# Kernel tuning notes

Hardware: AMD Instinct MI355X
Metric: run time of the kernel (lower is better)

Reference implementation:

```python
import jax, jax.numpy as jnp
import numpy as np

OUT_CHANNELS = 16
PH = PW = 7          # output_size
SR = 2               # sampling_ratio


def setup_inputs() -> dict:
    key = jax.random.key(0)
    k1, k2, k3, k4 = jax.random.split(key, 4)
    B, C, H, W = 4, OUT_CHANNELS * PH * PW, 80, 80
    feat = jax.random.normal(k1, (B, C, H, W), dtype=jnp.float32)
    N = 512
    bidx = jax.random.randint(k2, (N,), 0, B).astype(jnp.float32)
    tl = jax.random.uniform(k3, (N, 2), minval=0.0, maxval=0.7)   # x1, y1 (normalized)
    sz = jax.random.uniform(k4, (N, 2), minval=0.05, maxval=0.3)  # box size
    rois = jnp.concatenate([bidx[:, None], tl, tl + sz], axis=1)  # [N,5]
    return {"input": feat, "rois": rois}


def _psroi_one(feat_ps, roi):
    # feat_ps: [B, Co, PH, PW, H, W]  (position-sensitive channel layout)
    B, Co, _, _, H, W = feat_ps.shape
    f = feat_ps[roi[0].astype(jnp.int32)]              # [Co, PH, PW, H, W]
    x1 = roi[1] * W; y1 = roi[2] * H
    x2 = roi[3] * W; y2 = roi[4] * H                   # adaptive spatial_scale = (H, W)
    roi_h = jnp.maximum(y2 - y1, 0.1)
    roi_w = jnp.maximum(x2 - x1, 0.1)
    bin_h = roi_h / PH
    bin_w = roi_w / PW
    # sample coordinates per bin: [PH,SR] and [PW,SR]
    ys = y1 + jnp.arange(PH, dtype=f.dtype)[:, None] * bin_h + (jnp.arange(SR, dtype=f.dtype)[None, :] + 0.5) * bin_h / SR
    xs = x1 + jnp.arange(PW, dtype=f.dtype)[:, None] * bin_w + (jnp.arange(SR, dtype=f.dtype)[None, :] + 0.5) * bin_w / SR
    ym = (ys >= -1.0) & (ys <= H)
    xm = (xs >= -1.0) & (xs <= W)
    yc = jnp.clip(ys, 0.0, H - 1)
    xc = jnp.clip(xs, 0.0, W - 1)
    y0 = jnp.floor(yc).astype(jnp.int32)
    x0 = jnp.floor(xc).astype(jnp.int32)
    y1i = jnp.minimum(y0 + 1, H - 1)
    x1i = jnp.minimum(x0 + 1, W - 1)
    ly = yc - y0.astype(f.dtype); hy = 1.0 - ly        # [PH,SR]
    lx = xc - x0.astype(f.dtype); hx = 1.0 - lx        # [PW,SR]
    I = jnp.arange(PH)[:, None, None, None]            # bin row index
    J = jnp.arange(PW)[None, None, :, None]            # bin col index

    def g(Y, X):
        # gather f[c, i, j, Y[i,sy], X[j,sx]] -> [Co, PH, SR, PW, SR]
        return f[:, I, J, Y[:, :, None, None], X[None, None, :, :]]

    v = (g(y0, x0)  * (hy[:, :, None, None] * hx[None, None])
       + g(y0, x1i) * (hy[:, :, None, None] * lx[None, None])
       + g(y1i, x0) * (ly[:, :, None, None] * hx[None, None])
       + g(y1i, x1i) * (ly[:, :, None, None] * lx[None, None]))
    v = v * (ym[:, :, None, None] & xm[None, None]).astype(v.dtype)
    return v.mean(axis=(2, 4))                          # [Co, PH, PW]


def reference(input, rois):
    B, C, H, W = input.shape
    feat_ps = input.reshape(B, OUT_CHANNELS, PH, PW, H, W)
    rois = rois.reshape(-1, 5)
    out = jax.vmap(lambda r: _psroi_one(feat_ps, r))(rois)  # [N, Co, PH, PW]
    return out
```

## Files before the change

kernel.cpp:

```cpp
#include <hip/hip_runtime.h>

#define NB   4
#define CO   16
#define PH   7
#define PW   7
#define SR   2
#define HH   80
#define WW   80
#define NROI 512
#define CIJ  (CO*PH*PW)
#define PLANE (HH*WW)
#define NF4  (PLANE/4)

typedef float f4v __attribute__((ext_vector_type(4), aligned(16)));

#define WS_ORDER_OFF 64
#define WS_GEOM_OFF  2048

__global__ __launch_bounds__(512) void psroi_prep_kernel(
    const float* __restrict__ rois, int* __restrict__ base,
    unsigned short* __restrict__ order, f4v* __restrict__ geom)
{
    __shared__ int cnt[NB];
    __shared__ int cbase[NB + 1];
    int n = threadIdx.x;
    if (n < NB) cnt[n] = 0;
    __syncthreads();
    int b = (int)rois[n * 5 + 0];
    int rank = atomicAdd(&cnt[b], 1);
    __syncthreads();
    if (n == 0) {
        cbase[0] = 0;
        for (int k = 0; k < NB; ++k) cbase[k + 1] = cbase[k] + cnt[k];
        for (int k = 0; k <= NB; ++k) base[k] = cbase[k];
    }
    __syncthreads();
    int pos = cbase[b] + rank;
    order[pos] = (unsigned short)n;

    float x1 = rois[n * 5 + 1] * (float)WW;
    float y1 = rois[n * 5 + 2] * (float)HH;
    float x2 = rois[n * 5 + 3] * (float)WW;
    float y2 = rois[n * 5 + 4] * (float)HH;
    f4v g;
    g.x = x1;
    g.y = y1;
    g.z = fmaxf(x2 - x1, 0.1f) * (1.0f / PW);
    g.w = fmaxf(y2 - y1, 0.1f) * (1.0f / PH);
    geom[pos] = g;
}

__global__ __launch_bounds__(256) void psroi_main_kernel(
    const float* __restrict__ feat,
    const int* __restrict__ base,
    const unsigned short* __restrict__ order,
    const f4v* __restrict__ geom,
    float* __restrict__ out)
{
    __shared__ __align__(16) float sp[PLANE];

    int u   = blockIdx.x;
    int cij = u >> 2;
    int b   = u & 3;
    int rem = cij % (PH * PW);
    int i = rem / PW;
    int j = rem % PW;
    int n = threadIdx.x;

    const f4v* src = (const f4v*)(feat + ((size_t)b * CIJ + (size_t)cij) * PLANE);
    f4v* dst = (f4v*)sp;
    #pragma unroll
    for (int it = 0; it < 6; ++it)
        dst[it * 256 + n] = src[it * 256 + n];
    {
        int e = 1536 + n;
        if (e < NF4) dst[e] = src[e];
    }

    int lo = base[b];
    int hi = base[b + 1];

    __syncthreads();

    for (int t = lo + n; t < hi; t += 256) {
        int m = (int)order[t];
        f4v g = geom[t];
        float x1 = g.x, y1 = g.y, bin_w = g.z, bin_h = g.w;

        float acc = 0.0f;
        #pragma unroll
        for (int sy = 0; sy < SR; ++sy) {
            float ys = y1 + (float)i * bin_h + ((float)sy + 0.5f) * bin_h / (float)SR;
            bool ymask = (ys >= -1.0f) && (ys <= (float)HH);
            float yc = fminf(fmaxf(ys, 0.0f), (float)(HH - 1));
            int   y0 = (int)floorf(yc);
            int   y1i = min(y0 + 1, HH - 1);
            float ly = yc - (float)y0, hy = 1.0f - ly;
            #pragma unroll
            for (int sx = 0; sx < SR; ++sx) {
                float xs = x1 + (float)j * bin_w + ((float)sx + 0.5f) * bin_w / (float)SR;
                bool xmask = (xs >= -1.0f) && (xs <= (float)WW);
                float xc = fminf(fmaxf(xs, 0.0f), (float)(WW - 1));
                int   x0 = (int)floorf(xc);
                int   x0c = min(x0, WW - 2);
                bool  sh = (x0 != x0c);
                float lx = xc - (float)x0, hx = 1.0f - lx;

                float t0 = sp[y0  * WW + x0c], t1 = sp[y0  * WW + x0c + 1];
                float b0 = sp[y1i * WW + x0c], b1 = sp[y1i * WW + x0c + 1];

                float v00 = sh ? t1 : t0;
                float v10 = sh ? b1 : b0;
                float v = (v00 * hx + t1 * lx) * hy + (v10 * hx + b1 * lx) * ly;
                if (ymask && xmask) acc += v;
            }
        }
        out[(size_t)m * CIJ + cij] = acc * 0.25f;
    }
}

extern "C" void kernel_launch(void* const* d_in, const int* in_sizes, int n_in,
                              void* d_out, int out_size, void* d_ws, size_t ws_size,
                              hipStream_t stream)
{
    const float* feat = (const float*)d_in[0];
    const float* rois = (const float*)d_in[1];
    float* out = (float*)d_out;

    char* ws = (char*)d_ws;
    int* base = (int*)ws;
    unsigned short* order = (unsigned short*)(ws + WS_ORDER_OFF);
    f4v* geom = (f4v*)(ws + WS_GEOM_OFF);

    psroi_prep_kernel<<<1, NROI, 0, stream>>>(rois, base, order, geom);
    psroi_main_kernel<<<CIJ * NB, 256, 0, stream>>>(feat, base, order, geom, out);
}
```

Baseline: 112.3 us.

## Drop ROI bucketing prep kernel; each block scans all ROIs and filters by batch

Removes the separate prep kernel that sorted ROIs by batch index and precomputed geometry, so the whole operation is one launch. Each block now has every thread read two ROIs directly, compute geometry inline, and skip ROIs whose batch does not match the block's batch. This saves a kernel launch and the serialization between the two kernels. In exchange every block reads all 512 ROIs, and lanes whose ROI belongs to another batch sit idle, causing warp divergence.

```diff
diff --git a/kernel.cpp b/kernel.cpp
--- a/kernel.cpp
+++ b/kernel.cpp
@@ -14,47 +14,52 @@
 
 typedef float f4v __attribute__((ext_vector_type(4), aligned(16)));
 
-#define WS_ORDER_OFF 64
-#define WS_GEOM_OFF  2048
+__device__ __forceinline__ void psroi_one(
+    const float* __restrict__ sp,
+    float rb, float rx1, float ry1, float rx2, float ry2,
+    int b, int i, int j, int cij, int m, float* __restrict__ out)
+{
+    if ((int)rb != b) return;
 
-__global__ __launch_bounds__(512) void psroi_prep_kernel(
-    const float* __restrict__ rois, int* __restrict__ base,
-    unsigned short* __restrict__ order, f4v* __restrict__ geom)
-{
-    __shared__ int cnt[NB];
-    __shared__ int cbase[NB + 1];
-    int n = threadIdx.x;
-    if (n < NB) cnt[n] = 0;
-    __syncthreads();
-    int b = (int)rois[n * 5 + 0];
-    int rank = atomicAdd(&cnt[b], 1);
-    __syncthreads();
-    if (n == 0) {
-        cbase[0] = 0;
-        for (int k = 0; k < NB; ++k) cbase[k + 1] = cbase[k] + cnt[k];
-        for (int k = 0; k <= NB; ++k) base[k] = cbase[k];
+    float x1 = rx1 * (float)WW;
+    float y1 = ry1 * (float)HH;
+    float bin_w = fmaxf(rx2 * (float)WW - x1, 0.1f) * (1.0f / PW);
+    float bin_h = fmaxf(ry2 * (float)HH - y1, 0.1f) * (1.0f / PH);
+
+    float acc = 0.0f;
+    #pragma unroll
+    for (int sy = 0; sy < SR; ++sy) {
+        float ys = y1 + (float)i * bin_h + ((float)sy + 0.5f) * bin_h * (1.0f / SR);
+        bool ymask = (ys >= -1.0f) && (ys <= (float)HH);
+        float yc = fminf(fmaxf(ys, 0.0f), (float)(HH - 1));
+        int   y0 = (int)floorf(yc);
+        int   y1i = min(y0 + 1, HH - 1);
+        float ly = yc - (float)y0, hy = 1.0f - ly;
+        #pragma unroll
+        for (int sx = 0; sx < SR; ++sx) {
+            float xs = x1 + (float)j * bin_w + ((float)sx + 0.5f) * bin_w * (1.0f / SR);
+            bool xmask = (xs >= -1.0f) && (xs <= (float)WW);
+            float xc = fminf(fmaxf(xs, 0.0f), (float)(WW - 1));
+            int   x0 = (int)floorf(xc);
+            int   x0c = min(x0, WW - 2);
+            bool  sh = (x0 != x0c);
+            float lx = xc - (float)x0, hx = 1.0f - lx;
+
+            float t0 = sp[y0  * WW + x0c], t1 = sp[y0  * WW + x0c + 1];
+            float b0 = sp[y1i * WW + x0c], b1 = sp[y1i * WW + x0c + 1];
+
+            float v00 = sh ? t1 : t0;
+            float v10 = sh ? b1 : b0;
+            float v = (v00 * hx + t1 * lx) * hy + (v10 * hx + b1 * lx) * ly;
+            if (ymask && xmask) acc += v;
+        }
     }
-    __syncthreads();
-    int pos = cbase[b] + rank;
-    order[pos] = (unsigned short)n;
-
-    float x1 = rois[n * 5 + 1] * (float)WW;
-    float y1 = rois[n * 5 + 2] * (float)HH;
-    float x2 = rois[n * 5 + 3] * (float)WW;
-    float y2 = rois[n * 5 + 4] * (float)HH;
-    f4v g;
-    g.x = x1;
-    g.y = y1;
-    g.z = fmaxf(x2 - x1, 0.1f) * (1.0f / PW);
-    g.w = fmaxf(y2 - y1, 0.1f) * (1.0f / PH);
-    geom[pos] = g;
+    out[(size_t)m * CIJ + cij] = acc * 0.25f;
 }
 
 __global__ __launch_bounds__(256) void psroi_main_kernel(
     const float* __restrict__ feat,
-    const int* __restrict__ base,
-    const unsigned short* __restrict__ order,
-    const f4v* __restrict__ geom,
+    const float* __restrict__ rois,
     float* __restrict__ out)
 {
     __shared__ __align__(16) float sp[PLANE];
@@ -77,46 +82,15 @@
         if (e < NF4) dst[e] = src[e];
     }
 
-    int lo = base[b];
-    int hi = base[b + 1];
+    const float* rp0 = rois + (size_t)n * 5;
+    const float* rp1 = rois + ((size_t)n + 256) * 5;
+    float a0 = rp0[0], a1 = rp0[1], a2 = rp0[2], a3 = rp0[3], a4 = rp0[4];
+    float c0 = rp1[0], c1 = rp1[1], c2 = rp1[2], c3 = rp1[3], c4 = rp1[4];
 
     __syncthreads();
 
-    for (int t = lo + n; t < hi; t += 256) {
-        int m = (int)order[t];
-        f4v g = geom[t];
-        float x1 = g.x, y1 = g.y, bin_w = g.z, bin_h = g.w;
-
-        float acc = 0.0f;
-        #pragma unroll
-        for (int sy = 0; sy < SR; ++sy) {
-            float ys = y1 + (float)i * bin_h + ((float)sy + 0.5f) * bin_h / (float)SR;
-            bool ymask = (ys >= -1.0f) && (ys <= (float)HH);
-            float yc = fminf(fmaxf(ys, 0.0f), (float)(HH - 1));
-            int   y0 = (int)floorf(yc);
-            int   y1i = min(y0 + 1, HH - 1);
-            float ly = yc - (float)y0, hy = 1.0f - ly;
-            #pragma unroll
-            for (int sx = 0; sx < SR; ++sx) {
-                float xs = x1 + (float)j * bin_w + ((float)sx + 0.5f) * bin_w / (float)SR;
-                bool xmask = (xs >= -1.0f) && (xs <= (float)WW);
-                float xc = fminf(fmaxf(xs, 0.0f), (float)(WW - 1));
-                int   x0 = (int)floorf(xc);
-                int   x0c = min(x0, WW - 2);
-                bool  sh = (x0 != x0c);
-                float lx = xc - (float)x0, hx = 1.0f - lx;
-
-                float t0 = sp[y0  * WW + x0c], t1 = sp[y0  * WW + x0c + 1];
-                float b0 = sp[y1i * WW + x0c], b1 = sp[y1i * WW + x0c + 1];
-
-                float v00 = sh ? t1 : t0;
-                float v10 = sh ? b1 : b0;
-                float v = (v00 * hx + t1 * lx) * hy + (v10 * hx + b1 * lx) * ly;
-                if (ymask && xmask) acc += v;
-            }
-        }
-        out[(size_t)m * CIJ + cij] = acc * 0.25f;
-    }
+    psroi_one(sp, a0, a1, a2, a3, a4, b, i, j, cij, n,       out);
+    psroi_one(sp, c0, c1, c2, c3, c4, b, i, j, cij, n + 256, out);
 }
 
 extern "C" void kernel_launch(void* const* d_in, const int* in_sizes, int n_in,
@@ -126,12 +100,7 @@
     const float* feat = (const float*)d_in[0];
     const float* rois = (const float*)d_in[1];
     float* out = (float*)d_out;
+    (void)d_ws; (void)ws_size; (void)in_sizes; (void)n_in; (void)out_size;
 
-    char* ws = (char*)d_ws;
-    int* base = (int*)ws;
-    unsigned short* order = (unsigned short*)(ws + WS_ORDER_OFF);
-    f4v* geom = (f4v*)(ws + WS_GEOM_OFF);
-
-    psroi_prep_kernel<<<1, NROI, 0, stream>>>(rois, base, order, geom);
-    psroi_main_kernel<<<CIJ * NB, 256, 0, stream>>>(feat, base, order, geom, out);
+    psroi_main_kernel<<<CIJ * NB, 256, 0, stream>>>(feat, rois, out);
 }
```

New measurement: 111.1 us. No clear change (-1.1%).
